# Performance work log

Hardware: AMD Instinct MI355X
Metric: run time of the kernel (lower is better)

## Reference

```python
import jax, jax.numpy as jnp
from jax import lax
import numpy as np
import math

B, T, IN_DIM, HID = 2048, 20, 600, 1024


def setup_inputs() -> dict:
    key = jax.random.key(0)
    kx, k1, k2, k3, k4 = jax.random.split(key, 5)
    std = 1.0 / math.sqrt(HID)  # reset_parameters: uniform(-std, std)
    x = jax.random.normal(kx, (B, T, IN_DIM), dtype=jnp.float32)
    W_ih = jax.random.uniform(k1, (3 * HID, IN_DIM), minval=-std, maxval=std, dtype=jnp.float32)
    b_ih = jax.random.uniform(k2, (3 * HID,), minval=-std, maxval=std, dtype=jnp.float32)
    W_hh = jax.random.uniform(k3, (3 * HID, HID), minval=-std, maxval=std, dtype=jnp.float32)
    b_hh = jax.random.uniform(k4, (3 * HID,), minval=-std, maxval=std, dtype=jnp.float32)
    return {"x": x, "W_ih": W_ih, "b_ih": b_ih, "W_hh": W_hh, "b_hh": b_hh}


def reference(x, W_ih, b_ih, W_hh, b_hh):
    # x: [B, T, in_dim]; returns last hidden state [B, HID]
    batch = x.shape[0]
    hid = W_hh.shape[1]
    # Precompute input-side gate projections for all timesteps (same math as per-step Linear)
    gate_x = jnp.einsum('btd,gd->btg', x, W_ih) + b_ih  # [B, T, 3H]

    def step(h, gxt):
        gate_h = h @ W_hh.T + b_hh  # [B, 3H]
        i_r, i_i, i_n = jnp.split(gxt, 3, axis=1)
        h_r, h_i, h_n = jnp.split(gate_h, 3, axis=1)
        resetgate = jax.nn.sigmoid(i_r + h_r)
        inputgate = jax.nn.sigmoid(i_i + h_i)
        newgate = jnp.tanh(i_n + resetgate * h_n)
        hy = newgate + inputgate * (h - newgate)
        return hy, None

    h0 = jnp.zeros((batch, hid), dtype=x.dtype)
    hT, _ = lax.scan(step, h0, jnp.swapaxes(gate_x, 0, 1))  # scan over time [T, B, 3H]
    return hT
```

## Files before the change

### kernel.cpp

```cpp
#include <hip/hip_runtime.h>
#include <hip/hip_bf16.h>
#include <math.h>

#define HID   1024
#define IN_D  600
#define IN_DP 640
#define BATCH 2048
#define TSTEP 20
#define BT    (BATCH * TSTEP)
#define G3    3072

typedef __attribute__((ext_vector_type(8))) short bf16x8;
typedef __attribute__((ext_vector_type(4))) float f32x4;

#define GLB(p) ((const __attribute__((address_space(1))) void*)(p))
#define LDS(p) ((__attribute__((address_space(3))) void*)(p))

__device__ __forceinline__ short f2bf(float f) {
    __hip_bfloat16 b = __float2bfloat16(f);
    return *(short*)&b;
}
__device__ __forceinline__ float bf2f(short s) {
    __hip_bfloat16 b = *(__hip_bfloat16*)&s;
    return __bfloat162float(b);
}

__global__ __launch_bounds__(512) void gemm_input2(const short* __restrict__ X,
                                                   const short* __restrict__ Wih_r,
                                                   const float* __restrict__ b_ih,
                                                   short* __restrict__ gx) {
    __shared__ short LDSF[4 * 20480];

    const int id    = blockIdx.x;
    const int xcd   = id & 7;
    const int local = id >> 3;
    const int jsub  = local & 1;
    const int mblk  = local >> 1;
    const int j0 = (xcd * 2 + jsub) * 64;
    const int m0 = mblk * 128;

    const int tid  = threadIdx.x;
    const int wave = tid >> 6;
    const int lane = tid & 63;
    const int wm = (wave >> 2) * 64;
    const int jg = wave & 3;
    const int fm = lane & 15;
    const int fq = lane >> 4;

    const int srow8 = lane >> 3;
    const int sxor  = ((lane & 7) ^ srow8) * 8;

    const short* Wblk = Wih_r + (size_t)(j0 * 3) * IN_DP;

    f32x4 acc[4][3] = {};

    auto stage = [&](int kc, int bsel) {
        int k0 = kc * 64;
        short* base = LDSF + bsel * 20480;
#pragma unroll
        for (int i = 0; i < 2; ++i) {
            int row0 = wave * 16 + i * 8;
            const short* g = X + (size_t)(m0 + row0 + srow8) * IN_DP + k0 + sxor;
            __builtin_amdgcn_global_load_lds(GLB(g), LDS(base + row0 * 64), 16, 0, 0);
        }
#pragma unroll
        for (int i = 0; i < 3; ++i) {
            int row0 = wave * 24 + i * 8;
            const short* g = Wblk + (size_t)(row0 + srow8) * IN_DP + k0 + sxor;
            __builtin_amdgcn_global_load_lds(GLB(g), LDS(base + 8192 + row0 * 64), 16, 0, 0);
        }
    };

    stage(0, 0);
    stage(1, 1);

#pragma unroll
    for (int ic = 0; ic < 10; ++ic) {
        if (ic < 8) stage(ic + 2, (ic + 2) & 3);
        if (ic < 8)       asm volatile("s_waitcnt vmcnt(10)" : : : "memory");
        else if (ic == 8) asm volatile("s_waitcnt vmcnt(5)"  : : : "memory");
        else              asm volatile("s_waitcnt vmcnt(0)"  : : : "memory");
        __builtin_amdgcn_s_barrier();
        __builtin_amdgcn_sched_barrier(0);

        short* buf = LDSF + (ic & 3) * 20480;

#pragma unroll
        for (int kk = 0; kk < 2; ++kk) {
            bf16x8 af[4], bg[3];
            const int cbase = kk * 32 + fq * 8;
            const int csw = cbase ^ ((fm & 7) * 8);
#pragma unroll
            for (int mi = 0; mi < 4; ++mi)
                af[mi] = *(const bf16x8*)(&buf[(wm + mi * 16 + fm) * 64 + csw]);
#pragma unroll
            for (int g = 0; g < 3; ++g)
                bg[g] = *(const bf16x8*)(&buf[8192 + (jg * 48 + g * 16 + fm) * 64 + csw]);
            __builtin_amdgcn_s_setprio(1);
#pragma unroll
            for (int mi = 0; mi < 4; ++mi)
#pragma unroll
                for (int g = 0; g < 3; ++g)
                    acc[mi][g] = __builtin_amdgcn_mfma_f32_16x16x32_bf16(af[mi], bg[g], acc[mi][g], 0, 0, 0);
            __builtin_amdgcn_s_setprio(0);
        }
    }

    const int jl = j0 + jg * 16 + fm;
#pragma unroll
    for (int g = 0; g < 3; ++g) {
        float bias = b_ih[g * HID + jl];
#pragma unroll
        for (int mi = 0; mi < 4; ++mi) {
#pragma unroll
            for (int r = 0; r < 4; ++r) {
                int gm = m0 + wm + mi * 16 + fq * 4 + r;
                gx[(size_t)gm * G3 + g * HID + jl] = f2bf(acc[mi][g][r] + bias);
            }
        }
    }
}

__global__ __launch_bounds__(512) void gru_step(const short* __restrict__ hb_in,
                                                const short* __restrict__ Wr,
                                                const short* __restrict__ gx,
                                                const float* __restrict__ b_hh,
                                                short* __restrict__ hb_out,
                                                float* __restrict__ out,
                                                int t, int last) {
    __shared__ short LDSF[4 * 20480];

    const int id   = blockIdx.x;
    const int xcd  = id & 7;
    const int rest = id >> 3;
    const int jsub = rest & 1;
    const int mblk = rest >> 1;
    const int j0 = (xcd * 2 + jsub) * 64;
    const int m0 = mblk * 128;
    const int hchunk = j0 >> 6;

    const int tid  = threadIdx.x;
    const int wave = tid >> 6;
    const int lane = tid & 63;
    const int wm = (wave >> 2) * 64;
    const int jg = wave & 3;
    const int fm = lane & 15;
    const int fq = lane >> 4;

    const int srow8 = lane >> 3;
    const int sxor  = ((lane & 7) ^ srow8) * 8;

    const short* Wblk = Wr + (size_t)(j0 * 3) * HID;
    const short* gxt  = gx + (size_t)t * BATCH * G3;

    f32x4 acc[4][3] = {};
    short hsnap[4][4];

    auto stage = [&](int kc, int bsel) {
        int k0 = kc * 64;
        short* base = LDSF + bsel * 20480;
#pragma unroll
        for (int i = 0; i < 2; ++i) {
            int row0 = wave * 16 + i * 8;
            const short* g = hb_in + (size_t)(m0 + row0 + srow8) * HID + k0 + sxor;
            __builtin_amdgcn_global_load_lds(GLB(g), LDS(base + row0 * 64), 16, 0, 0);
        }
#pragma unroll
        for (int i = 0; i < 3; ++i) {
            int row0 = wave * 24 + i * 8;
            const short* g = Wblk + (size_t)(row0 + srow8) * HID + k0 + sxor;
            __builtin_amdgcn_global_load_lds(GLB(g), LDS(base + 8192 + row0 * 64), 16, 0, 0);
        }
    };
    auto sgx_load = [&](int q) {
        int g = q >> 4;
        int row0 = (q & 15) * 8;
        const short* src = gxt + (size_t)(m0 + row0 + srow8) * G3 + g * HID + j0 + sxor;
        __builtin_amdgcn_global_load_lds(GLB(src), LDS(LDSF + q * 512), 16, 0, 0);
    };

    const int jj = jg * 16 + fm;

    stage(0, 0);
    stage(1, 1);

#pragma unroll
    for (int ic = 0; ic < 16; ++ic) {
        if (ic < 14) {
            stage(ic + 2, (ic + 2) & 3);
        } else if (ic == 14) {
#pragma unroll
            for (int i = 0; i < 5; ++i) sgx_load(wave * 5 + i);
        } else {
            sgx_load(40 + wave);
        }
        if (ic < 15) asm volatile("s_waitcnt vmcnt(10)" : : : "memory");
        else         asm volatile("s_waitcnt vmcnt(6)"  : : : "memory");
        __builtin_amdgcn_s_barrier();
        __builtin_amdgcn_sched_barrier(0);

        short* buf = LDSF + (ic & 3) * 20480;

        if (ic == hchunk) {
#pragma unroll
            for (int mi = 0; mi < 4; ++mi)
#pragma unroll
                for (int r = 0; r < 4; ++r) {
                    int mrow = wm + mi * 16 + fq * 4 + r;
                    hsnap[mi][r] = buf[mrow * 64 + (jj ^ ((mrow & 7) * 8))];
                }
        }

#pragma unroll
        for (int kk = 0; kk < 2; ++kk) {
            bf16x8 af[4], bg[3];
            const int cbase = kk * 32 + fq * 8;
            const int csw = cbase ^ ((fm & 7) * 8);
#pragma unroll
            for (int mi = 0; mi < 4; ++mi)
                af[mi] = *(const bf16x8*)(&buf[(wm + mi * 16 + fm) * 64 + csw]);
#pragma unroll
            for (int g = 0; g < 3; ++g)
                bg[g] = *(const bf16x8*)(&buf[8192 + (jg * 48 + g * 16 + fm) * 64 + csw]);
            __builtin_amdgcn_s_setprio(1);
#pragma unroll
            for (int mi = 0; mi < 4; ++mi)
#pragma unroll
                for (int g = 0; g < 3; ++g)
                    acc[mi][g] = __builtin_amdgcn_mfma_f32_16x16x32_bf16(af[mi], bg[g], acc[mi][g], 0, 0, 0);
            __builtin_amdgcn_s_setprio(0);
        }
    }

    asm volatile("s_waitcnt vmcnt(0)" : : : "memory");
    __builtin_amdgcn_s_barrier();
    __builtin_amdgcn_sched_barrier(0);

    const short* sGX = LDSF;
    const int jlane = j0 + jj;
    const float bh_r = b_hh[jlane];
    const float bh_i = b_hh[HID + jlane];
    const float bh_n = b_hh[2 * HID + jlane];

#pragma unroll
    for (int mi = 0; mi < 4; ++mi) {
#pragma unroll
        for (int r = 0; r < 4; ++r) {
            int mloc = wm + mi * 16 + fq * 4 + r;
            int gm = m0 + mloc;
            int jsw = jj ^ ((mloc & 7) * 8);
            float xr = bf2f(sGX[        mloc * 64 + jsw]);
            float xi = bf2f(sGX[ 8192 + mloc * 64 + jsw]);
            float xn = bf2f(sGX[16384 + mloc * 64 + jsw]);

            float rg = 1.0f / (1.0f + __expf(-(xr + acc[mi][0][r] + bh_r)));
            float ig = 1.0f / (1.0f + __expf(-(xi + acc[mi][1][r] + bh_i)));
            float ng = tanhf(xn + rg * (acc[mi][2][r] + bh_n));

            float h  = bf2f(hsnap[mi][r]);
            float hy = ng + ig * (h - ng);
            size_t idx = (size_t)gm * HID + jlane;
            hb_out[idx] = f2bf(hy);
            if (last) out[idx] = hy;
        }
    }
}

__global__ __launch_bounds__(256) void cvt_x(const float* __restrict__ X, short* __restrict__ Xb) {
    int rd = blockIdx.x;
    int tt = rd >> 11;
    int b  = rd & (BATCH - 1);
    const float* s = X + ((size_t)b * TSTEP + tt) * IN_D;
    short* d = Xb + (size_t)rd * IN_DP;
    for (int c = threadIdx.x; c < IN_DP; c += 256)
        d[c] = (c < IN_D) ? f2bf(s[c]) : (short)0;
}

__global__ __launch_bounds__(256) void cvt_wih_r(const float* __restrict__ W, short* __restrict__ Wb) {
    int n  = blockIdx.x;
    int jb = n / 48;
    int rem = n - jb * 48;
    int g  = rem >> 4;
    int ji = rem & 15;
    const float* s = W + (size_t)(g * HID + jb * 16 + ji) * IN_D;
    short* d = Wb + (size_t)n * IN_DP;
    for (int c = threadIdx.x; c < IN_DP; c += 256)
        d[c] = (c < IN_D) ? f2bf(s[c]) : (short)0;
}

__global__ __launch_bounds__(256) void cvt_whh(const float* __restrict__ W, short* __restrict__ Wr) {
    int n  = blockIdx.x;
    int jb = n / 48;
    int rem = n - jb * 48;
    int g  = rem >> 4;
    int ji = rem & 15;
    const float* s = W + (size_t)(g * HID + jb * 16 + ji) * HID;
    short* d = Wr + (size_t)n * HID;
    for (int c = threadIdx.x; c < HID; c += 256) d[c] = f2bf(s[c]);
}

extern "C" void kernel_launch(void* const* d_in, const int* in_sizes, int n_in,
                              void* d_out, int out_size, void* d_ws, size_t ws_size,
                              hipStream_t stream) {
    const float* x    = (const float*)d_in[0];
    const float* W_ih = (const float*)d_in[1];
    const float* b_ih = (const float*)d_in[2];
    const float* W_hh = (const float*)d_in[3];
    const float* b_hh = (const float*)d_in[4];
    float* out = (float*)d_out;

    char* p = (char*)d_ws;
    short* gx     = (short*)p;  p += (size_t)BT * G3 * 2;
    short* x_bf   = (short*)p;  p += (size_t)BT * IN_DP * 2;
    short* hb0    = (short*)p;  p += (size_t)BATCH * HID * 2;
    short* hb1    = (short*)p;  p += (size_t)BATCH * HID * 2;
    short* Wih_r  = (short*)p;  p += (size_t)G3 * IN_DP * 2;
    short* Whh_r  = (short*)p;  p += (size_t)G3 * HID * 2;

    cvt_wih_r<<<G3, 256, 0, stream>>>(W_ih, Wih_r);
    cvt_whh<<<G3, 256, 0, stream>>>(W_hh, Whh_r);
    cvt_x<<<BT, 256, 0, stream>>>(x, x_bf);
    hipMemsetAsync(hb0, 0, (size_t)BATCH * HID * 2, stream);

    gemm_input2<<<5120, 512, 0, stream>>>(x_bf, Wih_r, b_ih, gx);

    for (int t = 0; t < TSTEP; ++t) {
        const short* hin = (t & 1) ? hb1 : hb0;
        short* hout      = (t & 1) ? hb0 : hb1;
        gru_step<<<256, 512, 0, stream>>>(hin, Whh_r, gx, b_hh,
                                          hout, out, t, t == TSTEP - 1 ? 1 : 0);
    }
}
```

Before: 795.1 us.

## Fuse all GRU timesteps into one persistent kernel with grid-wide atomic barriers

Replaces the 20 per-timestep gru_step launches with a single persistent gru_fused kernel. It loops over time and synchronises all 256 blocks through an atomic counter spin barrier between steps. Blocks claim work tiles through per-XCC atomic slot counters, so each XCD handles a contiguous batch range and reuses its L2. W_hh tiles are prefetched before the barrier so weight loads overlap the wait. This removes launch overhead and tail effects, at the cost of relying on all 256 blocks being co-resident and on correct memory visibility for the spin barrier (h loads use a cache-policy bit).

```diff
diff --git a/kernel.cpp b/kernel.cpp
--- a/kernel.cpp
+++ b/kernel.cpp
@@ -121,23 +121,14 @@
     }
 }
 
-__global__ __launch_bounds__(512) void gru_step(const short* __restrict__ hb_in,
-                                                const short* __restrict__ Wr,
-                                                const short* __restrict__ gx,
-                                                const float* __restrict__ b_hh,
-                                                short* __restrict__ hb_out,
-                                                float* __restrict__ out,
-                                                int t, int last) {
+__global__ __launch_bounds__(512) void gru_fused(short* hb0, short* hb1,
+                                                 const short* __restrict__ Wr,
+                                                 const short* __restrict__ gx,
+                                                 const float* __restrict__ b_hh,
+                                                 float* __restrict__ out,
+                                                 unsigned* __restrict__ cnt,
+                                                 unsigned* __restrict__ xslot) {
     __shared__ short LDSF[4 * 20480];
-
-    const int id   = blockIdx.x;
-    const int xcd  = id & 7;
-    const int rest = id >> 3;
-    const int jsub = rest & 1;
-    const int mblk = rest >> 1;
-    const int j0 = (xcd * 2 + jsub) * 64;
-    const int m0 = mblk * 128;
-    const int hchunk = j0 >> 6;
 
     const int tid  = threadIdx.x;
     const int wave = tid >> 6;
@@ -150,118 +141,163 @@
     const int srow8 = lane >> 3;
     const int sxor  = ((lane & 7) ^ srow8) * 8;
 
+    unsigned xcc;
+    asm volatile("s_getreg_b32 %0, hwreg(HW_REG_XCC_ID)" : "=s"(xcc));
+    if (tid == 0) {
+        unsigned s = __hip_atomic_fetch_add(&xslot[xcc & 7], 1u,
+                                            __ATOMIC_RELAXED,
+                                            __HIP_MEMORY_SCOPE_AGENT);
+        asm volatile("s_waitcnt vmcnt(0)" : : : "memory");
+        *(volatile int*)LDSF = (int)s;
+    }
+    __syncthreads();
+    const int slot = *(volatile int*)LDSF;
+    __syncthreads();
+
+    const int m0 = (int)(xcc & 7) * 256 + (slot >> 4) * 128;
+    const int j0 = (slot & 15) * 64;
+    const int hchunk = slot & 15;
+
     const short* Wblk = Wr + (size_t)(j0 * 3) * HID;
-    const short* gxt  = gx + (size_t)t * BATCH * G3;
-
-    f32x4 acc[4][3] = {};
-    short hsnap[4][4];
-
-    auto stage = [&](int kc, int bsel) {
-        int k0 = kc * 64;
-        short* base = LDSF + bsel * 20480;
-#pragma unroll
-        for (int i = 0; i < 2; ++i) {
-            int row0 = wave * 16 + i * 8;
-            const short* g = hb_in + (size_t)(m0 + row0 + srow8) * HID + k0 + sxor;
-            __builtin_amdgcn_global_load_lds(GLB(g), LDS(base + row0 * 64), 16, 0, 0);
-        }
-#pragma unroll
-        for (int i = 0; i < 3; ++i) {
-            int row0 = wave * 24 + i * 8;
-            const short* g = Wblk + (size_t)(row0 + srow8) * HID + k0 + sxor;
-            __builtin_amdgcn_global_load_lds(GLB(g), LDS(base + 8192 + row0 * 64), 16, 0, 0);
-        }
-    };
-    auto sgx_load = [&](int q) {
-        int g = q >> 4;
-        int row0 = (q & 15) * 8;
-        const short* src = gxt + (size_t)(m0 + row0 + srow8) * G3 + g * HID + j0 + sxor;
-        __builtin_amdgcn_global_load_lds(GLB(src), LDS(LDSF + q * 512), 16, 0, 0);
-    };
-
     const int jj = jg * 16 + fm;
-
-    stage(0, 0);
-    stage(1, 1);
-
-#pragma unroll
-    for (int ic = 0; ic < 16; ++ic) {
-        if (ic < 14) {
-            stage(ic + 2, (ic + 2) & 3);
-        } else if (ic == 14) {
-#pragma unroll
-            for (int i = 0; i < 5; ++i) sgx_load(wave * 5 + i);
-        } else {
-            sgx_load(40 + wave);
-        }
-        if (ic < 15) asm volatile("s_waitcnt vmcnt(10)" : : : "memory");
-        else         asm volatile("s_waitcnt vmcnt(6)"  : : : "memory");
-        __builtin_amdgcn_s_barrier();
-        __builtin_amdgcn_sched_barrier(0);
-
-        short* buf = LDSF + (ic & 3) * 20480;
-
-        if (ic == hchunk) {
-#pragma unroll
-            for (int mi = 0; mi < 4; ++mi)
-#pragma unroll
-                for (int r = 0; r < 4; ++r) {
-                    int mrow = wm + mi * 16 + fq * 4 + r;
-                    hsnap[mi][r] = buf[mrow * 64 + (jj ^ ((mrow & 7) * 8))];
-                }
-        }
-
-#pragma unroll
-        for (int kk = 0; kk < 2; ++kk) {
-            bf16x8 af[4], bg[3];
-            const int cbase = kk * 32 + fq * 8;
-            const int csw = cbase ^ ((fm & 7) * 8);
-#pragma unroll
-            for (int mi = 0; mi < 4; ++mi)
-                af[mi] = *(const bf16x8*)(&buf[(wm + mi * 16 + fm) * 64 + csw]);
-#pragma unroll
-            for (int g = 0; g < 3; ++g)
-                bg[g] = *(const bf16x8*)(&buf[8192 + (jg * 48 + g * 16 + fm) * 64 + csw]);
-            __builtin_amdgcn_s_setprio(1);
-#pragma unroll
-            for (int mi = 0; mi < 4; ++mi)
-#pragma unroll
-                for (int g = 0; g < 3; ++g)
-                    acc[mi][g] = __builtin_amdgcn_mfma_f32_16x16x32_bf16(af[mi], bg[g], acc[mi][g], 0, 0, 0);
-            __builtin_amdgcn_s_setprio(0);
-        }
-    }
-
-    asm volatile("s_waitcnt vmcnt(0)" : : : "memory");
-    __builtin_amdgcn_s_barrier();
-    __builtin_amdgcn_sched_barrier(0);
-
-    const short* sGX = LDSF;
     const int jlane = j0 + jj;
     const float bh_r = b_hh[jlane];
     const float bh_i = b_hh[HID + jlane];
     const float bh_n = b_hh[2 * HID + jlane];
 
-#pragma unroll
-    for (int mi = 0; mi < 4; ++mi) {
-#pragma unroll
-        for (int r = 0; r < 4; ++r) {
-            int mloc = wm + mi * 16 + fq * 4 + r;
-            int gm = m0 + mloc;
-            int jsw = jj ^ ((mloc & 7) * 8);
-            float xr = bf2f(sGX[        mloc * 64 + jsw]);
-            float xi = bf2f(sGX[ 8192 + mloc * 64 + jsw]);
-            float xn = bf2f(sGX[16384 + mloc * 64 + jsw]);
-
-            float rg = 1.0f / (1.0f + __expf(-(xr + acc[mi][0][r] + bh_r)));
-            float ig = 1.0f / (1.0f + __expf(-(xi + acc[mi][1][r] + bh_i)));
-            float ng = tanhf(xn + rg * (acc[mi][2][r] + bh_n));
-
-            float h  = bf2f(hsnap[mi][r]);
-            float hy = ng + ig * (h - ng);
-            size_t idx = (size_t)gm * HID + jlane;
-            hb_out[idx] = f2bf(hy);
-            if (last) out[idx] = hy;
+#pragma unroll 1
+    for (int t = 0; t < TSTEP; ++t) {
+        const short* hin  = (t & 1) ? hb1 : hb0;
+        short*       hout = (t & 1) ? hb0 : hb1;
+        const short* gxt  = gx + (size_t)t * BATCH * G3;
+
+        auto stageW = [&](int kc, int bsel) {
+            int k0 = kc * 64;
+            short* base = LDSF + bsel * 20480;
+#pragma unroll
+            for (int i = 0; i < 3; ++i) {
+                int row0 = wave * 24 + i * 8;
+                const short* g = Wblk + (size_t)(row0 + srow8) * HID + k0 + sxor;
+                __builtin_amdgcn_global_load_lds(GLB(g), LDS(base + 8192 + row0 * 64), 16, 0, 0);
+            }
+        };
+        auto stageH = [&](int kc, int bsel) {
+            int k0 = kc * 64;
+            short* base = LDSF + bsel * 20480;
+#pragma unroll
+            for (int i = 0; i < 2; ++i) {
+                int row0 = wave * 16 + i * 8;
+                const short* g = hin + (size_t)(m0 + row0 + srow8) * HID + k0 + sxor;
+                __builtin_amdgcn_global_load_lds(GLB(g), LDS(base + row0 * 64), 16, 0, 1);
+            }
+        };
+        auto stage = [&](int kc, int bsel) { stageH(kc, bsel); stageW(kc, bsel); };
+        auto sgx_load = [&](int q) {
+            int g = q >> 4;
+            int row0 = (q & 15) * 8;
+            const short* src = gxt + (size_t)(m0 + row0 + srow8) * G3 + g * HID + j0 + sxor;
+            __builtin_amdgcn_global_load_lds(GLB(src), LDS(LDSF + q * 512), 16, 0, 0);
+        };
+
+        stageW(0, 0);
+        stageW(1, 1);
+        if (t > 0) {
+            if (tid == 0) {
+                __hip_atomic_fetch_add(&cnt[t * 32], 1u, __ATOMIC_RELAXED,
+                                       __HIP_MEMORY_SCOPE_AGENT);
+                while (__hip_atomic_load(&cnt[t * 32], __ATOMIC_RELAXED,
+                                         __HIP_MEMORY_SCOPE_AGENT) < 256u)
+                    __builtin_amdgcn_s_sleep(2);
+                asm volatile("s_waitcnt vmcnt(0)" : : : "memory");
+            }
+            __syncthreads();
+        }
+        stageH(0, 0);
+        stageH(1, 1);
+
+        f32x4 acc[4][3] = {};
+        short hsnap[4][4];
+
+#pragma unroll
+        for (int ic = 0; ic < 16; ++ic) {
+            if (ic < 14) {
+                stage(ic + 2, (ic + 2) & 3);
+            } else if (ic == 14) {
+#pragma unroll
+                for (int i = 0; i < 5; ++i) sgx_load(wave * 5 + i);
+            } else {
+                sgx_load(40 + wave);
+            }
+            if (ic == 0)       asm volatile("s_waitcnt vmcnt(7)"  : : : "memory");
+            else if (ic < 15)  asm volatile("s_waitcnt vmcnt(10)" : : : "memory");
+            else               asm volatile("s_waitcnt vmcnt(6)"  : : : "memory");
+            __builtin_amdgcn_s_barrier();
+            __builtin_amdgcn_sched_barrier(0);
+
+            short* buf = LDSF + (ic & 3) * 20480;
+
+            if (ic == hchunk) {
+#pragma unroll
+                for (int mi = 0; mi < 4; ++mi)
+#pragma unroll
+                    for (int r = 0; r < 4; ++r) {
+                        int mrow = wm + mi * 16 + fq * 4 + r;
+                        hsnap[mi][r] = buf[mrow * 64 + (jj ^ ((mrow & 7) * 8))];
+                    }
+            }
+
+#pragma unroll
+            for (int kk = 0; kk < 2; ++kk) {
+                bf16x8 af[4], bg[3];
+                const int cbase = kk * 32 + fq * 8;
+                const int csw = cbase ^ ((fm & 7) * 8);
+#pragma unroll
+                for (int mi = 0; mi < 4; ++mi)
+                    af[mi] = *(const bf16x8*)(&buf[(wm + mi * 16 + fm) * 64 + csw]);
+#pragma unroll
+                for (int g = 0; g < 3; ++g)
+                    bg[g] = *(const bf16x8*)(&buf[8192 + (jg * 48 + g * 16 + fm) * 64 + csw]);
+                __builtin_amdgcn_s_setprio(1);
+#pragma unroll
+                for (int mi = 0; mi < 4; ++mi)
+#pragma unroll
+                    for (int g = 0; g < 3; ++g)
+                        acc[mi][g] = __builtin_amdgcn_mfma_f32_16x16x32_bf16(af[mi], bg[g], acc[mi][g], 0, 0, 0);
+                __builtin_amdgcn_s_setprio(0);
+            }
+        }
+
+        asm volatile("s_waitcnt vmcnt(0)" : : : "memory");
+        __builtin_amdgcn_s_barrier();
+        __builtin_amdgcn_sched_barrier(0);
+
+        const short* sGX = LDSF;
+#pragma unroll
+        for (int mi = 0; mi < 4; ++mi) {
+#pragma unroll
+            for (int r = 0; r < 4; ++r) {
+                int mloc = wm + mi * 16 + fq * 4 + r;
+                int gm = m0 + mloc;
+                int jsw = jj ^ ((mloc & 7) * 8);
+                float xr = bf2f(sGX[        mloc * 64 + jsw]);
+                float xi = bf2f(sGX[ 8192 + mloc * 64 + jsw]);
+                float xn = bf2f(sGX[16384 + mloc * 64 + jsw]);
+
+                float rg = 1.0f / (1.0f + __expf(-(xr + acc[mi][0][r] + bh_r)));
+                float ig = 1.0f / (1.0f + __expf(-(xi + acc[mi][1][r] + bh_i)));
+                float ng = tanhf(xn + rg * (acc[mi][2][r] + bh_n));
+
+                float h  = bf2f(hsnap[mi][r]);
+                float hy = ng + ig * (h - ng);
+                size_t idx = (size_t)gm * HID + jlane;
+                hout[idx] = f2bf(hy);
+                if (t == TSTEP - 1) out[idx] = hy;
+            }
+        }
+
+        if (t < TSTEP - 1) {
+            asm volatile("s_waitcnt vmcnt(0)" : : : "memory");
+            __syncthreads();
         }
     }
 }
@@ -316,18 +352,16 @@
     short* hb1    = (short*)p;  p += (size_t)BATCH * HID * 2;
     short* Wih_r  = (short*)p;  p += (size_t)G3 * IN_DP * 2;
     short* Whh_r  = (short*)p;  p += (size_t)G3 * HID * 2;
+    unsigned* cnt   = (unsigned*)p; p += 20 * 32 * 4;
+    unsigned* xslot = (unsigned*)p; p += 8 * 4;
 
     cvt_wih_r<<<G3, 256, 0, stream>>>(W_ih, Wih_r);
     cvt_whh<<<G3, 256, 0, stream>>>(W_hh, Whh_r);
     cvt_x<<<BT, 256, 0, stream>>>(x, x_bf);
     hipMemsetAsync(hb0, 0, (size_t)BATCH * HID * 2, stream);
+    hipMemsetAsync(cnt, 0, 20 * 32 * 4 + 8 * 4, stream);
 
     gemm_input2<<<5120, 512, 0, stream>>>(x_bf, Wih_r, b_ih, gx);
 
-    for (int t = 0; t < TSTEP; ++t) {
-        const short* hin = (t & 1) ? hb1 : hb0;
-        short* hout      = (t & 1) ? hb0 : hb1;
-        gru_step<<<256, 512, 0, stream>>>(hin, Whh_r, gx, b_hh,
-                                          hout, out, t, t == TSTEP - 1 ? 1 : 0);
-    }
-}
+    gru_fused<<<256, 512, 0, stream>>>(hb0, hb1, Whh_r, gx, b_hh, out, cnt, xslot);
+}
```

Result: slower. 1.185 ms (+49.1%).

## Load h operand directly from global into registers instead of via LDS staging

Applied to the files above, without the earlier changes.

The GRU step kernel no longer stages the hidden-state A tile through LDS. Each wave reads its h fragments straight from global memory into registers, while only W_hh tiles go through the LDS ring. The gate_x tile is now prefetched up front into a dedicated LDS region, and the wait counts are retuned to match. The aim is to cut LDS traffic and footprint, at the cost of uncoalesced global reads that sit on the MFMA critical path without latency hiding. The h value for the final update is also reloaded from global rather than snapshotted.

```diff
diff --git a/kernel.cpp b/kernel.cpp
--- a/kernel.cpp
+++ b/kernel.cpp
@@ -128,7 +128,7 @@
                                                 short* __restrict__ hb_out,
                                                 float* __restrict__ out,
                                                 int t, int last) {
-    __shared__ short LDSF[4 * 20480];
+    __shared__ short LDSF[4 * 12288 + 3 * 8192];
 
     const int id   = blockIdx.x;
     const int xcd  = id & 7;
@@ -137,7 +137,6 @@
     const int mblk = rest >> 1;
     const int j0 = (xcd * 2 + jsub) * 64;
     const int m0 = mblk * 128;
-    const int hchunk = j0 >> 6;
 
     const int tid  = threadIdx.x;
     const int wave = tid >> 6;
@@ -154,89 +153,79 @@
     const short* gxt  = gx + (size_t)t * BATCH * G3;
 
     f32x4 acc[4][3] = {};
-    short hsnap[4][4];
 
     auto stage = [&](int kc, int bsel) {
         int k0 = kc * 64;
-        short* base = LDSF + bsel * 20480;
-#pragma unroll
-        for (int i = 0; i < 2; ++i) {
-            int row0 = wave * 16 + i * 8;
-            const short* g = hb_in + (size_t)(m0 + row0 + srow8) * HID + k0 + sxor;
-            __builtin_amdgcn_global_load_lds(GLB(g), LDS(base + row0 * 64), 16, 0, 0);
-        }
+        short* base = LDSF + bsel * 12288;
 #pragma unroll
         for (int i = 0; i < 3; ++i) {
             int row0 = wave * 24 + i * 8;
             const short* g = Wblk + (size_t)(row0 + srow8) * HID + k0 + sxor;
-            __builtin_amdgcn_global_load_lds(GLB(g), LDS(base + 8192 + row0 * 64), 16, 0, 0);
+            __builtin_amdgcn_global_load_lds(GLB(g), LDS(base + row0 * 64), 16, 0, 0);
         }
     };
-    auto sgx_load = [&](int q) {
+
+    const short* hrow[4];
+#pragma unroll
+    for (int mi = 0; mi < 4; ++mi)
+        hrow[mi] = hb_in + (size_t)(m0 + wm + mi * 16 + fm) * HID + fq * 8;
+
+    const int jj = jg * 16 + fm;
+
+    stage(0, 0);
+    stage(1, 1);
+#pragma unroll
+    for (int i = 0; i < 6; ++i) {
+        int q = wave * 6 + i;
         int g = q >> 4;
         int row0 = (q & 15) * 8;
         const short* src = gxt + (size_t)(m0 + row0 + srow8) * G3 + g * HID + j0 + sxor;
-        __builtin_amdgcn_global_load_lds(GLB(src), LDS(LDSF + q * 512), 16, 0, 0);
-    };
-
-    const int jj = jg * 16 + fm;
-
-    stage(0, 0);
-    stage(1, 1);
+        __builtin_amdgcn_global_load_lds(GLB(src), LDS(LDSF + 49152 + q * 512), 16, 0, 0);
+    }
 
 #pragma unroll
     for (int ic = 0; ic < 16; ++ic) {
-        if (ic < 14) {
-            stage(ic + 2, (ic + 2) & 3);
-        } else if (ic == 14) {
-#pragma unroll
-            for (int i = 0; i < 5; ++i) sgx_load(wave * 5 + i);
-        } else {
-            sgx_load(40 + wave);
-        }
-        if (ic < 15) asm volatile("s_waitcnt vmcnt(10)" : : : "memory");
-        else         asm volatile("s_waitcnt vmcnt(6)"  : : : "memory");
+        if (ic < 14) stage(ic + 2, (ic + 2) & 3);
+        if (ic < 2)       asm volatile("s_waitcnt vmcnt(12)" : : : "memory");
+        else if (ic < 14) asm volatile("s_waitcnt vmcnt(6)"  : : : "memory");
+        else if (ic == 14) asm volatile("s_waitcnt vmcnt(3)" : : : "memory");
+        else               asm volatile("s_waitcnt vmcnt(0)" : : : "memory");
         __builtin_amdgcn_s_barrier();
         __builtin_amdgcn_sched_barrier(0);
 
-        short* buf = LDSF + (ic & 3) * 20480;
-
-        if (ic == hchunk) {
-#pragma unroll
-            for (int mi = 0; mi < 4; ++mi)
-#pragma unroll
-                for (int r = 0; r < 4; ++r) {
-                    int mrow = wm + mi * 16 + fq * 4 + r;
-                    hsnap[mi][r] = buf[mrow * 64 + (jj ^ ((mrow & 7) * 8))];
-                }
-        }
+        short* buf = LDSF + (ic & 3) * 12288;
+        const int k0 = ic * 64;
+
+        bf16x8 af0[4], af1[4];
+#pragma unroll
+        for (int mi = 0; mi < 4; ++mi) {
+            af0[mi] = *(const bf16x8*)(hrow[mi] + k0);
+            af1[mi] = *(const bf16x8*)(hrow[mi] + k0 + 32);
+        }
+        __builtin_amdgcn_sched_barrier(0);
 
 #pragma unroll
         for (int kk = 0; kk < 2; ++kk) {
-            bf16x8 af[4], bg[3];
+            bf16x8 bg[3];
             const int cbase = kk * 32 + fq * 8;
             const int csw = cbase ^ ((fm & 7) * 8);
 #pragma unroll
+            for (int g = 0; g < 3; ++g)
+                bg[g] = *(const bf16x8*)(&buf[(jg * 48 + g * 16 + fm) * 64 + csw]);
+            __builtin_amdgcn_s_setprio(1);
+#pragma unroll
             for (int mi = 0; mi < 4; ++mi)
-                af[mi] = *(const bf16x8*)(&buf[(wm + mi * 16 + fm) * 64 + csw]);
-#pragma unroll
-            for (int g = 0; g < 3; ++g)
-                bg[g] = *(const bf16x8*)(&buf[8192 + (jg * 48 + g * 16 + fm) * 64 + csw]);
-            __builtin_amdgcn_s_setprio(1);
-#pragma unroll
-            for (int mi = 0; mi < 4; ++mi)
 #pragma unroll
                 for (int g = 0; g < 3; ++g)
-                    acc[mi][g] = __builtin_amdgcn_mfma_f32_16x16x32_bf16(af[mi], bg[g], acc[mi][g], 0, 0, 0);
+                    acc[mi][g] = __builtin_amdgcn_mfma_f32_16x16x32_bf16(
+                        kk ? af1[mi] : af0[mi], bg[g], acc[mi][g], 0, 0, 0);
             __builtin_amdgcn_s_setprio(0);
         }
     }
 
-    asm volatile("s_waitcnt vmcnt(0)" : : : "memory");
     __builtin_amdgcn_s_barrier();
-    __builtin_amdgcn_sched_barrier(0);
-
-    const short* sGX = LDSF;
+
+    const short* sGX = LDSF + 49152;
     const int jlane = j0 + jj;
     const float bh_r = b_hh[jlane];
     const float bh_i = b_hh[HID + jlane];
@@ -257,7 +246,7 @@
             float ig = 1.0f / (1.0f + __expf(-(xi + acc[mi][1][r] + bh_i)));
             float ng = tanhf(xn + rg * (acc[mi][2][r] + bh_n));
 
-            float h  = bf2f(hsnap[mi][r]);
+            float h  = bf2f(hb_in[(size_t)gm * HID + jlane]);
             float hy = ng + ig * (h - ng);
             size_t idx = (size_t)gm * HID + jlane;
             hb_out[idx] = f2bf(hy);
```

Measured after the change: 1.369 ms. 1.72x slower.

## Make input GEMM persistent across M-tiles and vectorize conversion kernels

Applied to the files above, without the earlier changes.

The input-projection GEMM now launches 256 persistent blocks. Each block loops over 20 M-tiles and prefetches the next tile's first K-chunks while the current tile's tail is computed, so the pipeline stays full across tiles instead of refilling in each of 5120 blocks. Bias loads are hoisted out of the tile loop. Separately, the fp32-to-bf16 conversion kernels now use float4 loads and short4 stores with a thread per 4 elements. The risk is less parallelism on the GPU and the epilogue stores now sitting on the critical path of each tile.

```diff
diff --git a/kernel.cpp b/kernel.cpp
--- a/kernel.cpp
+++ b/kernel.cpp
@@ -12,6 +12,8 @@
 
 typedef __attribute__((ext_vector_type(8))) short bf16x8;
 typedef __attribute__((ext_vector_type(4))) float f32x4;
+typedef __attribute__((ext_vector_type(4))) float fl4;
+typedef __attribute__((ext_vector_type(4))) short sh4;
 
 #define GLB(p) ((const __attribute__((address_space(1))) void*)(p))
 #define LDS(p) ((__attribute__((address_space(3))) void*)(p))
@@ -25,19 +27,17 @@
     return __bfloat162float(b);
 }
 
-__global__ __launch_bounds__(512) void gemm_input2(const short* __restrict__ X,
+__global__ __launch_bounds__(512) void gemm_input3(const short* __restrict__ X,
                                                    const short* __restrict__ Wih_r,
                                                    const float* __restrict__ b_ih,
                                                    short* __restrict__ gx) {
     __shared__ short LDSF[4 * 20480];
 
-    const int id    = blockIdx.x;
-    const int xcd   = id & 7;
-    const int local = id >> 3;
-    const int jsub  = local & 1;
-    const int mblk  = local >> 1;
+    const int id   = blockIdx.x;
+    const int xcd  = id & 7;
+    const int jsub = (id >> 3) & 1;
+    const int mgrp = id >> 4;
     const int j0 = (xcd * 2 + jsub) * 64;
-    const int m0 = mblk * 128;
 
     const int tid  = threadIdx.x;
     const int wave = tid >> 6;
@@ -52,9 +52,7 @@
 
     const short* Wblk = Wih_r + (size_t)(j0 * 3) * IN_DP;
 
-    f32x4 acc[4][3] = {};
-
-    auto stage = [&](int kc, int bsel) {
+    auto stage_m = [&](int m0, int kc, int bsel) {
         int k0 = kc * 64;
         short* base = LDSF + bsel * 20480;
 #pragma unroll
@@ -71,53 +69,80 @@
         }
     };
 
-    stage(0, 0);
-    stage(1, 1);
-
-#pragma unroll
-    for (int ic = 0; ic < 10; ++ic) {
-        if (ic < 8) stage(ic + 2, (ic + 2) & 3);
-        if (ic < 8)       asm volatile("s_waitcnt vmcnt(10)" : : : "memory");
-        else if (ic == 8) asm volatile("s_waitcnt vmcnt(5)"  : : : "memory");
-        else              asm volatile("s_waitcnt vmcnt(0)"  : : : "memory");
-        __builtin_amdgcn_s_barrier();
-        __builtin_amdgcn_sched_barrier(0);
-
-        short* buf = LDSF + (ic & 3) * 20480;
-
-#pragma unroll
-        for (int kk = 0; kk < 2; ++kk) {
-            bf16x8 af[4], bg[3];
-            const int cbase = kk * 32 + fq * 8;
-            const int csw = cbase ^ ((fm & 7) * 8);
-#pragma unroll
-            for (int mi = 0; mi < 4; ++mi)
-                af[mi] = *(const bf16x8*)(&buf[(wm + mi * 16 + fm) * 64 + csw]);
+    const int jl = j0 + jg * 16 + fm;
+    const float bias0 = b_ih[jl];
+    const float bias1 = b_ih[HID + jl];
+    const float bias2 = b_ih[2 * HID + jl];
+
+    f32x4 acc[4][3] = {};
+
+    stage_m(mgrp * 128, 0, 0);
+    stage_m(mgrp * 128, 1, 1);
+
+    int cc = 0;
+#pragma unroll 1
+    for (int mt = 0; mt < 20; ++mt) {
+        const int m0cur = (mgrp + 16 * mt) * 128;
+        const int m0nxt = (mgrp + 16 * (mt + 1)) * 128;
+
+#pragma unroll
+        for (int kc = 0; kc < 10; ++kc) {
+            if (kc < 8)        stage_m(m0cur, kc + 2, (cc + kc + 2) & 3);
+            else if (mt < 19)  stage_m(m0nxt, kc - 8, (cc + kc + 2) & 3);
+
+            if (kc < 8) {
+                asm volatile("s_waitcnt vmcnt(10)" : : : "memory");
+            } else if (mt < 19) {
+                asm volatile("s_waitcnt vmcnt(10)" : : : "memory");
+            } else if (kc == 8) {
+                asm volatile("s_waitcnt vmcnt(5)"  : : : "memory");
+            } else {
+                asm volatile("s_waitcnt vmcnt(0)"  : : : "memory");
+            }
+            __builtin_amdgcn_s_barrier();
+            __builtin_amdgcn_sched_barrier(0);
+
+            short* buf = LDSF + ((cc + kc) & 3) * 20480;
+
+#pragma unroll
+            for (int kk = 0; kk < 2; ++kk) {
+                bf16x8 af[4], bg[3];
+                const int cbase = kk * 32 + fq * 8;
+                const int csw = cbase ^ ((fm & 7) * 8);
+#pragma unroll
+                for (int mi = 0; mi < 4; ++mi)
+                    af[mi] = *(const bf16x8*)(&buf[(wm + mi * 16 + fm) * 64 + csw]);
+#pragma unroll
+                for (int g = 0; g < 3; ++g)
+                    bg[g] = *(const bf16x8*)(&buf[8192 + (jg * 48 + g * 16 + fm) * 64 + csw]);
+                __builtin_amdgcn_s_setprio(1);
+#pragma unroll
+                for (int mi = 0; mi < 4; ++mi)
+#pragma unroll
+                    for (int g = 0; g < 3; ++g)
+                        acc[mi][g] = __builtin_amdgcn_mfma_f32_16x16x32_bf16(af[mi], bg[g], acc[mi][g], 0, 0, 0);
+                __builtin_amdgcn_s_setprio(0);
+            }
+        }
+
+#pragma unroll
+        for (int mi = 0; mi < 4; ++mi) {
+#pragma unroll
+            for (int r = 0; r < 4; ++r) {
+                int gm = m0cur + wm + mi * 16 + fq * 4 + r;
+                size_t rowb = (size_t)gm * G3;
+                gx[rowb + jl]            = f2bf(acc[mi][0][r] + bias0);
+                gx[rowb + HID + jl]      = f2bf(acc[mi][1][r] + bias1);
+                gx[rowb + 2 * HID + jl]  = f2bf(acc[mi][2][r] + bias2);
+            }
+        }
+#pragma unroll
+        for (int mi = 0; mi < 4; ++mi)
 #pragma unroll
             for (int g = 0; g < 3; ++g)
-                bg[g] = *(const bf16x8*)(&buf[8192 + (jg * 48 + g * 16 + fm) * 64 + csw]);
-            __builtin_amdgcn_s_setprio(1);
-#pragma unroll
-            for (int mi = 0; mi < 4; ++mi)
-#pragma unroll
-                for (int g = 0; g < 3; ++g)
-                    acc[mi][g] = __builtin_amdgcn_mfma_f32_16x16x32_bf16(af[mi], bg[g], acc[mi][g], 0, 0, 0);
-            __builtin_amdgcn_s_setprio(0);
-        }
-    }
-
-    const int jl = j0 + jg * 16 + fm;
-#pragma unroll
-    for (int g = 0; g < 3; ++g) {
-        float bias = b_ih[g * HID + jl];
-#pragma unroll
-        for (int mi = 0; mi < 4; ++mi) {
-#pragma unroll
-            for (int r = 0; r < 4; ++r) {
-                int gm = m0 + wm + mi * 16 + fq * 4 + r;
-                gx[(size_t)gm * G3 + g * HID + jl] = f2bf(acc[mi][g][r] + bias);
-            }
-        }
+                acc[mi][g] = (f32x4){0.f, 0.f, 0.f, 0.f};
+
+        cc += 10;
     }
 }
 
@@ -266,17 +291,23 @@
     }
 }
 
-__global__ __launch_bounds__(256) void cvt_x(const float* __restrict__ X, short* __restrict__ Xb) {
+__global__ __launch_bounds__(192) void cvt_x(const float* __restrict__ X, short* __restrict__ Xb) {
     int rd = blockIdx.x;
     int tt = rd >> 11;
     int b  = rd & (BATCH - 1);
     const float* s = X + ((size_t)b * TSTEP + tt) * IN_D;
     short* d = Xb + (size_t)rd * IN_DP;
-    for (int c = threadIdx.x; c < IN_DP; c += 256)
-        d[c] = (c < IN_D) ? f2bf(s[c]) : (short)0;
-}
-
-__global__ __launch_bounds__(256) void cvt_wih_r(const float* __restrict__ W, short* __restrict__ Wb) {
+    int c = threadIdx.x;
+    if (c < 150) {
+        fl4 v = *(const fl4*)(s + c * 4);
+        sh4 o = { f2bf(v[0]), f2bf(v[1]), f2bf(v[2]), f2bf(v[3]) };
+        *(sh4*)(d + c * 4) = o;
+    } else if (c < 160) {
+        *(sh4*)(d + c * 4) = (sh4){0, 0, 0, 0};
+    }
+}
+
+__global__ __launch_bounds__(192) void cvt_wih_r(const float* __restrict__ W, short* __restrict__ Wb) {
     int n  = blockIdx.x;
     int jb = n / 48;
     int rem = n - jb * 48;
@@ -284,8 +315,14 @@
     int ji = rem & 15;
     const float* s = W + (size_t)(g * HID + jb * 16 + ji) * IN_D;
     short* d = Wb + (size_t)n * IN_DP;
-    for (int c = threadIdx.x; c < IN_DP; c += 256)
-        d[c] = (c < IN_D) ? f2bf(s[c]) : (short)0;
+    int c = threadIdx.x;
+    if (c < 150) {
+        fl4 v = *(const fl4*)(s + c * 4);
+        sh4 o = { f2bf(v[0]), f2bf(v[1]), f2bf(v[2]), f2bf(v[3]) };
+        *(sh4*)(d + c * 4) = o;
+    } else if (c < 160) {
+        *(sh4*)(d + c * 4) = (sh4){0, 0, 0, 0};
+    }
 }
 
 __global__ __launch_bounds__(256) void cvt_whh(const float* __restrict__ W, short* __restrict__ Wr) {
@@ -296,7 +333,10 @@
     int ji = rem & 15;
     const float* s = W + (size_t)(g * HID + jb * 16 + ji) * HID;
     short* d = Wr + (size_t)n * HID;
-    for (int c = threadIdx.x; c < HID; c += 256) d[c] = f2bf(s[c]);
+    int c = threadIdx.x;
+    fl4 v = *(const fl4*)(s + c * 4);
+    sh4 o = { f2bf(v[0]), f2bf(v[1]), f2bf(v[2]), f2bf(v[3]) };
+    *(sh4*)(d + c * 4) = o;
 }
 
 extern "C" void kernel_launch(void* const* d_in, const int* in_sizes, int n_in,
@@ -317,12 +357,12 @@
     short* Wih_r  = (short*)p;  p += (size_t)G3 * IN_DP * 2;
     short* Whh_r  = (short*)p;  p += (size_t)G3 * HID * 2;
 
-    cvt_wih_r<<<G3, 256, 0, stream>>>(W_ih, Wih_r);
+    cvt_wih_r<<<G3, 192, 0, stream>>>(W_ih, Wih_r);
     cvt_whh<<<G3, 256, 0, stream>>>(W_hh, Whh_r);
-    cvt_x<<<BT, 256, 0, stream>>>(x, x_bf);
+    cvt_x<<<BT, 192, 0, stream>>>(x, x_bf);
     hipMemsetAsync(hb0, 0, (size_t)BATCH * HID * 2, stream);
 
-    gemm_input2<<<5120, 512, 0, stream>>>(x_bf, Wih_r, b_ih, gx);
+    gemm_input3<<<256, 512, 0, stream>>>(x_bf, Wih_r, b_ih, gx);
 
     for (int t = 0; t < TSTEP; ++t) {
         const short* hin = (t & 1) ? hb1 : hb0;
```

New measurement: 734.2 us. 1.08x faster.
